# Performance work log

Measured on AMD Instinct MI355X. Metric: run time of the kernel, lower is better.

The kernel has to match this reference:

```python
import jax, jax.numpy as jnp
import numpy as np

V, E, H, D, S = 50257, 512, 512, 1024, 1024


def _gru_final(x_seq, Wih, Whh, bih, bhh):
    """Run a torch-style GRUCell over x_seq [S,E] from h0=0; return final hidden [H]."""
    h_dim = Whh.shape[1]
    gi = x_seq @ Wih.T + bih  # [S,3H] input-side gates, precomputed

    def step(h, g):
        gh = Whh @ h + bhh  # [3H]
        r = jax.nn.sigmoid(g[:h_dim] + gh[:h_dim])
        z = jax.nn.sigmoid(g[h_dim:2 * h_dim] + gh[h_dim:2 * h_dim])
        n = jnp.tanh(g[2 * h_dim:] + r * gh[2 * h_dim:])
        h_new = (1.0 - z) * n + z * h
        return h_new, None

    h_final, _ = jax.lax.scan(step, jnp.zeros((h_dim,), x_seq.dtype), gi)
    return h_final


def _bidir_encode(x_seq, Wih_f, Whh_f, bih_f, bhh_f, Wih_b, Whh_b, bih_b, bhh_b):
    hf = _gru_final(x_seq, Wih_f, Whh_f, bih_f, bhh_f)
    hb = _gru_final(x_seq[::-1], Wih_b, Whh_b, bih_b, bhh_b)
    return jnp.concatenate([hf, hb])  # [2H]


def setup_inputs() -> dict:
    key = jax.random.key(0)
    ks = jax.random.split(key, 32)
    inp = {"sentence": jax.random.randint(ks[0], (S,), 0, V, dtype=jnp.int64)}
    inp["emb"] = jax.random.normal(ks[1], (V, E), jnp.float32) * 0.1
    i = 2
    for pre in ["ctx_f", "ctx_b", "qry_f", "qry_b"]:
        inp[pre + "_Wih"] = jax.random.normal(ks[i], (3 * H, E), jnp.float32) * 0.02; i += 1
        inp[pre + "_Whh"] = jax.random.normal(ks[i], (3 * H, H), jnp.float32) * 0.02; i += 1
        inp[pre + "_bih"] = jax.random.normal(ks[i], (3 * H,), jnp.float32) * 0.02; i += 1
        inp[pre + "_bhh"] = jax.random.normal(ks[i], (3 * H,), jnp.float32) * 0.02; i += 1
    inp["d1_w"] = jax.random.normal(ks[i], (D, 4 * H), jnp.float32) * 0.02; i += 1
    inp["d1_b"] = jnp.zeros((D,), jnp.float32)
    inp["d2_w"] = jax.random.normal(ks[i], (1, D), jnp.float32) * 0.02
    inp["d2_b"] = jnp.zeros((1,), jnp.float32)
    return inp


def reference(sentence, emb,
              ctx_f_Wih, ctx_f_Whh, ctx_f_bih, ctx_f_bhh,
              ctx_b_Wih, ctx_b_Whh, ctx_b_bih, ctx_b_bhh,
              qry_f_Wih, qry_f_Whh, qry_f_bih, qry_f_bhh,
              qry_b_Wih, qry_b_Whh, qry_b_bih, qry_b_bhh,
              d1_w, d1_b, d2_w, d2_b):
    # Embedding lookup (dropout = identity in eval mode)
    x_seq = emb[sentence]  # [S,E]
    ctx = _bidir_encode(x_seq, ctx_f_Wih, ctx_f_Whh, ctx_f_bih, ctx_f_bhh,
                        ctx_b_Wih, ctx_b_Whh, ctx_b_bih, ctx_b_bhh)  # [2H]
    qry = _bidir_encode(x_seq, qry_f_Wih, qry_f_Whh, qry_f_bih, qry_f_bhh,
                        qry_b_Wih, qry_b_Whh, qry_b_bih, qry_b_bhh)  # [2H]
    rep = jnp.concatenate([ctx, qry])  # [4H]
    h1 = jax.nn.relu(rep @ d1_w.T + d1_b)  # [D]
    return jax.nn.sigmoid(h1 @ d2_w.T + d2_b)  # [1]
```

## Files before the change

kernel.cpp:

```cpp
#include <hip/hip_runtime.h>
#include <math.h>

typedef unsigned long long u64;

#define S_LEN 1024
#define E_DIM 512
#define H_DIM 512
#define G3    1536
#define D_DIM 1024

#define NCHAIN 4
#define WPC    32

#define TM 64
#define TN 64
#define BK 32

__global__ __launch_bounds__(256) void gi_gemm_kernel(
    const int* __restrict__ sent, const float* __restrict__ emb,
    const float* __restrict__ Wih0, const float* __restrict__ bih0,
    const float* __restrict__ Wih1, const float* __restrict__ bih1,
    const float* __restrict__ Wih2, const float* __restrict__ bih2,
    const float* __restrict__ Wih3, const float* __restrict__ bih3,
    float* __restrict__ gi)
{
    __shared__ float As[BK][TM + 1];
    __shared__ float Bs[BK][TN + 1];
    __shared__ int   rows[TM];

    const int blocks_t = S_LEN / TM;
    const int blocks_j = G3 / TN;
    int b   = blockIdx.x;
    int p   = b / (blocks_t * blocks_j);
    int rem = b % (blocks_t * blocks_j);
    int bt  = rem / blocks_j;
    int bj  = rem % blocks_j;

    const float* Wih = (p == 0) ? Wih0 : (p == 1) ? Wih1 : (p == 2) ? Wih2 : Wih3;
    const float* bih = (p == 0) ? bih0 : (p == 1) ? bih1 : (p == 2) ? bih2 : bih3;

    int tid = threadIdx.x;
    if (tid < TM) rows[tid] = sent[bt * TM + tid];
    __syncthreads();

    int tt = (tid >> 4) * 4;
    int jj = (tid & 15) * 4;
    float acc[4][4] = {{0.f}};

    int lr = tid >> 2;
    int lc = (tid & 3) * 8;

    for (int k0 = 0; k0 < E_DIM; k0 += BK) {
        const float* asrc = emb + (size_t)rows[lr] * E_DIM + (k0 + lc);
        float4 a0 = *(const float4*)asrc;
        float4 a1 = *(const float4*)(asrc + 4);
        const float* bsrc = Wih + (size_t)(bj * TN + lr) * E_DIM + (k0 + lc);
        float4 b0 = *(const float4*)bsrc;
        float4 b1 = *(const float4*)(bsrc + 4);

        As[lc+0][lr]=a0.x; As[lc+1][lr]=a0.y; As[lc+2][lr]=a0.z; As[lc+3][lr]=a0.w;
        As[lc+4][lr]=a1.x; As[lc+5][lr]=a1.y; As[lc+6][lr]=a1.z; As[lc+7][lr]=a1.w;
        Bs[lc+0][lr]=b0.x; Bs[lc+1][lr]=b0.y; Bs[lc+2][lr]=b0.z; Bs[lc+3][lr]=b0.w;
        Bs[lc+4][lr]=b1.x; Bs[lc+5][lr]=b1.y; Bs[lc+6][lr]=b1.z; Bs[lc+7][lr]=b1.w;
        __syncthreads();

        #pragma unroll
        for (int kk = 0; kk < BK; ++kk) {
            float av[4], bv[4];
            #pragma unroll
            for (int e = 0; e < 4; ++e) { av[e] = As[kk][tt+e]; bv[e] = Bs[kk][jj+e]; }
            #pragma unroll
            for (int i = 0; i < 4; ++i)
                #pragma unroll
                for (int j2 = 0; j2 < 4; ++j2)
                    acc[i][j2] = fmaf(av[i], bv[j2], acc[i][j2]);
        }
        __syncthreads();
    }

    float* gout = gi + (size_t)p * S_LEN * G3;
    int jbase = bj * TN + jj;
    float bb0 = bih[jbase+0], bb1 = bih[jbase+1], bb2 = bih[jbase+2], bb3 = bih[jbase+3];
    #pragma unroll
    for (int i = 0; i < 4; ++i) {
        int t = bt * TM + tt + i;
        float4 v = make_float4(acc[i][0]+bb0, acc[i][1]+bb1, acc[i][2]+bb2, acc[i][3]+bb3);
        *(float4*)(gout + (size_t)t * G3 + jbase) = v;
    }
}

__device__ __forceinline__ float fast_sigmoid(float x) {
    return __builtin_amdgcn_rcpf(1.f + __expf(-x));
}
__device__ __forceinline__ float fast_tanh(float x) {
    return 1.f - 2.f * __builtin_amdgcn_rcpf(1.f + __expf(2.f * x));
}

__global__ __launch_bounds__(256, 1) void gru_scan_kernel(
    const float* __restrict__ Whh0, const float* __restrict__ bhh0,
    const float* __restrict__ Whh1, const float* __restrict__ bhh1,
    const float* __restrict__ Whh2, const float* __restrict__ bhh2,
    const float* __restrict__ Whh3, const float* __restrict__ bhh3,
    const float* __restrict__ gi,
    u64* __restrict__ hpk)
{
    __shared__ float lds_h[2][H_DIM];

    int b = blockIdx.x;
    int c = b / WPC;
    int w = b % WPC;
    const float* Whh = (c==0)?Whh0:(c==1)?Whh1:(c==2)?Whh2:Whh3;
    const float* bhh = (c==0)?bhh0:(c==1)?bhh1:(c==2)?bhh2:bhh3;
    const float* gic = gi + (size_t)c * S_LEN * G3;
    u64* hp = hpk + (size_t)c * 2 * H_DIM;
    const bool fwd = ((c & 1) == 0);

    int tid  = threadIdx.x;
    int wv   = tid >> 6;
    int lane = tid & 63;
    int q    = lane >> 4;
    int r    = lane & 15;
    int base_i = w * 16 + wv * 4;
    int my_i   = base_i + q;
    bool pub   = (r == 0);

    float4 wregv[3][8];
    #pragma unroll
    for (int g = 0; g < 3; ++g) {
        const float* rowp = Whh + (size_t)(g * H_DIM + my_i) * H_DIM;
        #pragma unroll
        for (int k = 0; k < 8; ++k)
            wregv[g][k] = *(const float4*)(rowp + 4 * r + 64 * k);
    }

    float bh_r=0.f, bh_z=0.f, bh_n=0.f;
    float gr=0.f, gz=0.f, gn=0.f;
    if (pub) {
        bh_r = bhh[my_i]; bh_z = bhh[H_DIM + my_i]; bh_n = bhh[2*H_DIM + my_i];
        int t0 = fwd ? 0 : (S_LEN - 1);
        const float* g0 = gic + (size_t)t0 * G3;
        gr = g0[my_i]; gz = g0[H_DIM + my_i]; gn = g0[2*H_DIM + my_i];
    }

    lds_h[0][tid]       = 0.f;
    lds_h[0][tid + 256] = 0.f;

    int s0 = tid, s1 = tid + 256;
    bool own0 = ((s0 >> 4) == w);
    bool own1 = ((s1 >> 4) == w);

    for (int s = 0; s < S_LEN; ++s) {
        int pb = s & 1;
        if (s > 0) {
            const u64* srcp = hp + (size_t)pb * H_DIM;
            bool p0 = own0, p1 = own1;
            while (!(p0 && p1)) {
                if (!p0) {
                    u64 v = __hip_atomic_load(srcp + s0, __ATOMIC_RELAXED, __HIP_MEMORY_SCOPE_AGENT);
                    if ((unsigned)(v >> 32) == (unsigned)s) {
                        lds_h[pb][s0] = __uint_as_float((unsigned)v);
                        p0 = true;
                    }
                }
                if (!p1) {
                    u64 v = __hip_atomic_load(srcp + s1, __ATOMIC_RELAXED, __HIP_MEMORY_SCOPE_AGENT);
                    if ((unsigned)(v >> 32) == (unsigned)s) {
                        lds_h[pb][s1] = __uint_as_float((unsigned)v);
                        p1 = true;
                    }
                }
            }
        }
        __syncthreads();

        float ngr = 0.f, ngz = 0.f, ngn = 0.f;
        if (pub && s + 1 < S_LEN) {
            int tn = fwd ? (s + 1) : (S_LEN - 2 - s);
            const float* gnx = gic + (size_t)tn * G3;
            ngr = gnx[my_i]; ngz = gnx[H_DIM + my_i]; ngn = gnx[2*H_DIM + my_i];
        }

        float hv = lds_h[pb][my_i];

        float4 hfv[8];
        const float* hbase = &lds_h[pb][0];
        #pragma unroll
        for (int k = 0; k < 8; ++k)
            hfv[k] = *(const float4*)(hbase + 4 * r + 64 * k);

        float acc[3];
        #pragma unroll
        for (int g = 0; g < 3; ++g) {
            float a = 0.f;
            #pragma unroll
            for (int k = 0; k < 8; ++k) {
                a = fmaf(wregv[g][k].x, hfv[k].x, a);
                a = fmaf(wregv[g][k].y, hfv[k].y, a);
                a = fmaf(wregv[g][k].z, hfv[k].z, a);
                a = fmaf(wregv[g][k].w, hfv[k].w, a);
            }
            acc[g] = a;
        }
        #pragma unroll
        for (int off = 8; off >= 1; off >>= 1)
            #pragma unroll
            for (int g = 0; g < 3; ++g)
                acc[g] += __shfl_down(acc[g], off, 16);

        if (pub) {
            float rr = fast_sigmoid(gr + acc[0] + bh_r);
            float zz = fast_sigmoid(gz + acc[1] + bh_z);
            float nn = fast_tanh(gn + rr * (acc[2] + bh_n));
            float hn = (1.f - zz) * nn + zz * hv;
            lds_h[pb ^ 1][my_i] = hn;
            union { float f; unsigned u; } cv; cv.f = hn;
            u64 pk = ((u64)(unsigned)(s + 1) << 32) | (u64)cv.u;
            __hip_atomic_store(hp + (size_t)(pb ^ 1) * H_DIM + my_i, pk,
                               __ATOMIC_RELAXED, __HIP_MEMORY_SCOPE_AGENT);
            gr = ngr; gz = ngz; gn = ngn;
        }
    }
}

__global__ __launch_bounds__(256) void dense1_kernel(
    const float* __restrict__ d1w, const float* __restrict__ d1b,
    const u64* __restrict__ hpk, float* __restrict__ h1)
{
    int wv = threadIdx.x >> 6, lane = threadIdx.x & 63;
    int row = blockIdx.x * 4 + wv;
    const float* wr = d1w + (size_t)row * (4 * H_DIM);
    float sum = 0.f;
    #pragma unroll
    for (int q = 0; q < 32; ++q) {
        int j = lane + q * 64;
        int cc = j >> 9;
        float h = __uint_as_float((unsigned)hpk[(size_t)cc * 2 * H_DIM + (j & 511)]);
        sum = fmaf(wr[j], h, sum);
    }
    #pragma unroll
    for (int off = 32; off >= 1; off >>= 1) sum += __shfl_xor(sum, off, 64);
    if (lane == 0) h1[row] = fmaxf(sum + d1b[row], 0.f);
}

__global__ __launch_bounds__(256) void dense2_kernel(
    const float* __restrict__ d2w, const float* __restrict__ d2b,
    const float* __restrict__ h1, float* __restrict__ out)
{
    __shared__ float red[4];
    int tid = threadIdx.x, lane = tid & 63, wv = tid >> 6;
    float sum = 0.f;
    #pragma unroll
    for (int q = 0; q < 4; ++q) { int j = tid + q * 256; sum = fmaf(d2w[j], h1[j], sum); }
    #pragma unroll
    for (int off = 32; off >= 1; off >>= 1) sum += __shfl_xor(sum, off, 64);
    if (lane == 0) red[wv] = sum;
    __syncthreads();
    if (tid == 0) {
        float t = red[0] + red[1] + red[2] + red[3] + d2b[0];
        out[0] = 1.f / (1.f + expf(-t));
    }
}

extern "C" void kernel_launch(void* const* d_in, const int* in_sizes, int n_in,
                              void* d_out, int out_size, void* d_ws, size_t ws_size,
                              hipStream_t stream) {
    const int*   sent = (const int*)d_in[0];
    const float* emb  = (const float*)d_in[1];
    const float* Wih[4], *Whh[4], *bih[4], *bhh[4];
    for (int p = 0; p < 4; ++p) {
        Wih[p] = (const float*)d_in[2 + 4*p + 0];
        Whh[p] = (const float*)d_in[2 + 4*p + 1];
        bih[p] = (const float*)d_in[2 + 4*p + 2];
        bhh[p] = (const float*)d_in[2 + 4*p + 3];
    }
    const float* d1w = (const float*)d_in[18];
    const float* d1b = (const float*)d_in[19];
    const float* d2w = (const float*)d_in[20];
    const float* d2b = (const float*)d_in[21];
    float* out = (float*)d_out;

    float* gi  = (float*)d_ws;
    u64*   hpk = (u64*)((char*)d_ws + (size_t)NCHAIN * S_LEN * G3 * sizeof(float));
    float* h1  = (float*)((char*)hpk + (size_t)NCHAIN * 2 * H_DIM * sizeof(u64));

    gi_gemm_kernel<<<NCHAIN * (S_LEN/TM) * (G3/TN), 256, 0, stream>>>(
        sent, emb,
        Wih[0], bih[0], Wih[1], bih[1], Wih[2], bih[2], Wih[3], bih[3], gi);

    gru_scan_kernel<<<NCHAIN * WPC, 256, 0, stream>>>(
        Whh[0], bhh[0], Whh[1], bhh[1], Whh[2], bhh[2], Whh[3], bhh[3],
        gi, hpk);

    dense1_kernel<<<D_DIM / 4, 256, 0, stream>>>(d1w, d1b, hpk, h1);
    dense2_kernel<<<1, 256, 0, stream>>>(d2w, d2b, h1, out);
}
```

Before: 2.267 ms.

## Fuse input-gate GEMM into the GRU scan, overlapping it with the spin-wait

Removes the separate input-projection GEMM kernel and its large gi workspace. Each scan block now keeps its slice of Wih in registers next to Whh, and computes the input-gate dot products for each step while it polls for the previous hidden state. The embedding row for the next step is prefetched into a double-buffered LDS buffer. In exchange, register pressure doubles (48 float4 weight vectors per thread), each step gains an extra __syncthreads, and the serial scan does more arithmetic per step.

```diff
diff --git a/kernel.cpp b/kernel.cpp
--- a/kernel.cpp
+++ b/kernel.cpp
@@ -12,106 +12,42 @@
 #define NCHAIN 4
 #define WPC    32
 
-#define TM 64
-#define TN 64
-#define BK 32
-
-__global__ __launch_bounds__(256) void gi_gemm_kernel(
-    const int* __restrict__ sent, const float* __restrict__ emb,
-    const float* __restrict__ Wih0, const float* __restrict__ bih0,
-    const float* __restrict__ Wih1, const float* __restrict__ bih1,
-    const float* __restrict__ Wih2, const float* __restrict__ bih2,
-    const float* __restrict__ Wih3, const float* __restrict__ bih3,
-    float* __restrict__ gi)
-{
-    __shared__ float As[BK][TM + 1];
-    __shared__ float Bs[BK][TN + 1];
-    __shared__ int   rows[TM];
-
-    const int blocks_t = S_LEN / TM;
-    const int blocks_j = G3 / TN;
-    int b   = blockIdx.x;
-    int p   = b / (blocks_t * blocks_j);
-    int rem = b % (blocks_t * blocks_j);
-    int bt  = rem / blocks_j;
-    int bj  = rem % blocks_j;
-
-    const float* Wih = (p == 0) ? Wih0 : (p == 1) ? Wih1 : (p == 2) ? Wih2 : Wih3;
-    const float* bih = (p == 0) ? bih0 : (p == 1) ? bih1 : (p == 2) ? bih2 : bih3;
-
-    int tid = threadIdx.x;
-    if (tid < TM) rows[tid] = sent[bt * TM + tid];
-    __syncthreads();
-
-    int tt = (tid >> 4) * 4;
-    int jj = (tid & 15) * 4;
-    float acc[4][4] = {{0.f}};
-
-    int lr = tid >> 2;
-    int lc = (tid & 3) * 8;
-
-    for (int k0 = 0; k0 < E_DIM; k0 += BK) {
-        const float* asrc = emb + (size_t)rows[lr] * E_DIM + (k0 + lc);
-        float4 a0 = *(const float4*)asrc;
-        float4 a1 = *(const float4*)(asrc + 4);
-        const float* bsrc = Wih + (size_t)(bj * TN + lr) * E_DIM + (k0 + lc);
-        float4 b0 = *(const float4*)bsrc;
-        float4 b1 = *(const float4*)(bsrc + 4);
-
-        As[lc+0][lr]=a0.x; As[lc+1][lr]=a0.y; As[lc+2][lr]=a0.z; As[lc+3][lr]=a0.w;
-        As[lc+4][lr]=a1.x; As[lc+5][lr]=a1.y; As[lc+6][lr]=a1.z; As[lc+7][lr]=a1.w;
-        Bs[lc+0][lr]=b0.x; Bs[lc+1][lr]=b0.y; Bs[lc+2][lr]=b0.z; Bs[lc+3][lr]=b0.w;
-        Bs[lc+4][lr]=b1.x; Bs[lc+5][lr]=b1.y; Bs[lc+6][lr]=b1.z; Bs[lc+7][lr]=b1.w;
-        __syncthreads();
-
-        #pragma unroll
-        for (int kk = 0; kk < BK; ++kk) {
-            float av[4], bv[4];
-            #pragma unroll
-            for (int e = 0; e < 4; ++e) { av[e] = As[kk][tt+e]; bv[e] = Bs[kk][jj+e]; }
-            #pragma unroll
-            for (int i = 0; i < 4; ++i)
-                #pragma unroll
-                for (int j2 = 0; j2 < 4; ++j2)
-                    acc[i][j2] = fmaf(av[i], bv[j2], acc[i][j2]);
-        }
-        __syncthreads();
-    }
-
-    float* gout = gi + (size_t)p * S_LEN * G3;
-    int jbase = bj * TN + jj;
-    float bb0 = bih[jbase+0], bb1 = bih[jbase+1], bb2 = bih[jbase+2], bb3 = bih[jbase+3];
-    #pragma unroll
-    for (int i = 0; i < 4; ++i) {
-        int t = bt * TM + tt + i;
-        float4 v = make_float4(acc[i][0]+bb0, acc[i][1]+bb1, acc[i][2]+bb2, acc[i][3]+bb3);
-        *(float4*)(gout + (size_t)t * G3 + jbase) = v;
-    }
-}
-
 __device__ __forceinline__ float fast_sigmoid(float x) {
     return __builtin_amdgcn_rcpf(1.f + __expf(-x));
 }
 __device__ __forceinline__ float fast_tanh(float x) {
     return 1.f - 2.f * __builtin_amdgcn_rcpf(1.f + __expf(2.f * x));
 }
-
-__global__ __launch_bounds__(256, 1) void gru_scan_kernel(
-    const float* __restrict__ Whh0, const float* __restrict__ bhh0,
-    const float* __restrict__ Whh1, const float* __restrict__ bhh1,
-    const float* __restrict__ Whh2, const float* __restrict__ bhh2,
-    const float* __restrict__ Whh3, const float* __restrict__ bhh3,
-    const float* __restrict__ gi,
+__device__ __forceinline__ float dot4(float4 a, float4 b, float acc) {
+    acc = fmaf(a.x, b.x, acc);
+    acc = fmaf(a.y, b.y, acc);
+    acc = fmaf(a.z, b.z, acc);
+    acc = fmaf(a.w, b.w, acc);
+    return acc;
+}
+
+__global__ __launch_bounds__(256, 1) void gru_scan_fused_kernel(
+    const int* __restrict__ sent, const float* __restrict__ emb,
+    const float* __restrict__ Wih0, const float* __restrict__ Whh0,
+    const float* __restrict__ bih0, const float* __restrict__ bhh0,
+    const float* __restrict__ Wih1, const float* __restrict__ Whh1,
+    const float* __restrict__ bih1, const float* __restrict__ bhh1,
+    const float* __restrict__ Wih2, const float* __restrict__ Whh2,
+    const float* __restrict__ bih2, const float* __restrict__ bhh2,
+    const float* __restrict__ Wih3, const float* __restrict__ Whh3,
+    const float* __restrict__ bih3, const float* __restrict__ bhh3,
     u64* __restrict__ hpk)
 {
     __shared__ float lds_h[2][H_DIM];
+    __shared__ float lds_x[2][E_DIM];
 
     int b = blockIdx.x;
     int c = b / WPC;
     int w = b % WPC;
+    const float* Wih = (c==0)?Wih0:(c==1)?Wih1:(c==2)?Wih2:Wih3;
     const float* Whh = (c==0)?Whh0:(c==1)?Whh1:(c==2)?Whh2:Whh3;
+    const float* bih = (c==0)?bih0:(c==1)?bih1:(c==2)?bih2:bih3;
     const float* bhh = (c==0)?bhh0:(c==1)?bhh1:(c==2)?bhh2:bhh3;
-    const float* gic = gi + (size_t)c * S_LEN * G3;
     u64* hp = hpk + (size_t)c * 2 * H_DIM;
     const bool fwd = ((c & 1) == 0);
 
@@ -124,26 +60,35 @@
     int my_i   = base_i + q;
     bool pub   = (r == 0);
 
-    float4 wregv[3][8];
+    float4 whr[3][8], wir[3][8];
     #pragma unroll
     for (int g = 0; g < 3; ++g) {
-        const float* rowp = Whh + (size_t)(g * H_DIM + my_i) * H_DIM;
+        const float* hrow = Whh + (size_t)(g * H_DIM + my_i) * H_DIM;
+        const float* irow = Wih + (size_t)(g * H_DIM + my_i) * E_DIM;
         #pragma unroll
-        for (int k = 0; k < 8; ++k)
-            wregv[g][k] = *(const float4*)(rowp + 4 * r + 64 * k);
+        for (int k = 0; k < 8; ++k) {
+            whr[g][k] = *(const float4*)(hrow + 4 * r + 64 * k);
+            wir[g][k] = *(const float4*)(irow + 4 * r + 64 * k);
+        }
     }
 
     float bh_r=0.f, bh_z=0.f, bh_n=0.f;
-    float gr=0.f, gz=0.f, gn=0.f;
+    float bi_r=0.f, bi_z=0.f, bi_n=0.f;
     if (pub) {
         bh_r = bhh[my_i]; bh_z = bhh[H_DIM + my_i]; bh_n = bhh[2*H_DIM + my_i];
-        int t0 = fwd ? 0 : (S_LEN - 1);
-        const float* g0 = gic + (size_t)t0 * G3;
-        gr = g0[my_i]; gz = g0[H_DIM + my_i]; gn = g0[2*H_DIM + my_i];
+        bi_r = bih[my_i]; bi_z = bih[H_DIM + my_i]; bi_n = bih[2*H_DIM + my_i];
     }
 
     lds_h[0][tid]       = 0.f;
     lds_h[0][tid + 256] = 0.f;
+    {
+        int t0 = fwd ? 0 : (S_LEN - 1);
+        int row0 = sent[t0];
+        if (tid < 128)
+            *(float4*)&lds_x[0][tid * 4] =
+                *(const float4*)(emb + (size_t)row0 * E_DIM + tid * 4);
+    }
+    __syncthreads();
 
     int s0 = tid, s1 = tid + 256;
     bool own0 = ((s0 >> 4) == w);
@@ -151,74 +96,87 @@
 
     for (int s = 0; s < S_LEN; ++s) {
         int pb = s & 1;
+        const float* xb = &lds_x[pb][0];
+        float ea0 = 0.f, ea1 = 0.f, ea2 = 0.f;
+        int ac = 0;
+
         if (s > 0) {
             const u64* srcp = hp + (size_t)pb * H_DIM;
             bool p0 = own0, p1 = own1;
             while (!(p0 && p1)) {
-                if (!p0) {
-                    u64 v = __hip_atomic_load(srcp + s0, __ATOMIC_RELAXED, __HIP_MEMORY_SCOPE_AGENT);
-                    if ((unsigned)(v >> 32) == (unsigned)s) {
-                        lds_h[pb][s0] = __uint_as_float((unsigned)v);
-                        p0 = true;
-                    }
+                u64 v0 = 0, v1 = 0;
+                if (!p0) v0 = __hip_atomic_load(srcp + s0, __ATOMIC_RELAXED, __HIP_MEMORY_SCOPE_AGENT);
+                if (!p1) v1 = __hip_atomic_load(srcp + s1, __ATOMIC_RELAXED, __HIP_MEMORY_SCOPE_AGENT);
+                if (ac < 8) {
+                    float4 xv = *(const float4*)(xb + 4 * r + 64 * ac);
+                    ea0 = dot4(wir[0][ac], xv, ea0);
+                    ea1 = dot4(wir[1][ac], xv, ea1);
+                    ea2 = dot4(wir[2][ac], xv, ea2);
+                    ++ac;
                 }
-                if (!p1) {
-                    u64 v = __hip_atomic_load(srcp + s1, __ATOMIC_RELAXED, __HIP_MEMORY_SCOPE_AGENT);
-                    if ((unsigned)(v >> 32) == (unsigned)s) {
-                        lds_h[pb][s1] = __uint_as_float((unsigned)v);
-                        p1 = true;
-                    }
+                if (!p0 && (unsigned)(v0 >> 32) == (unsigned)s) {
+                    lds_h[pb][s0] = __uint_as_float((unsigned)v0);
+                    p0 = true;
+                }
+                if (!p1 && (unsigned)(v1 >> 32) == (unsigned)s) {
+                    lds_h[pb][s1] = __uint_as_float((unsigned)v1);
+                    p1 = true;
                 }
             }
         }
+        for (; ac < 8; ++ac) {
+            float4 xv = *(const float4*)(xb + 4 * r + 64 * ac);
+            ea0 = dot4(wir[0][ac], xv, ea0);
+            ea1 = dot4(wir[1][ac], xv, ea1);
+            ea2 = dot4(wir[2][ac], xv, ea2);
+        }
         __syncthreads();
 
-        float ngr = 0.f, ngz = 0.f, ngn = 0.f;
-        if (pub && s + 1 < S_LEN) {
+        float4 xpre = make_float4(0.f, 0.f, 0.f, 0.f);
+        bool do_pre = (tid < 128) && (s + 1 < S_LEN);
+        if (do_pre) {
             int tn = fwd ? (s + 1) : (S_LEN - 2 - s);
-            const float* gnx = gic + (size_t)tn * G3;
-            ngr = gnx[my_i]; ngz = gnx[H_DIM + my_i]; ngn = gnx[2*H_DIM + my_i];
+            int rown = sent[tn];
+            xpre = *(const float4*)(emb + (size_t)rown * E_DIM + tid * 4);
         }
 
         float hv = lds_h[pb][my_i];
 
-        float4 hfv[8];
-        const float* hbase = &lds_h[pb][0];
+        float ha0 = 0.f, ha1 = 0.f, ha2 = 0.f;
+        const float* hb = &lds_h[pb][0];
         #pragma unroll
-        for (int k = 0; k < 8; ++k)
-            hfv[k] = *(const float4*)(hbase + 4 * r + 64 * k);
-
-        float acc[3];
+        for (int k = 0; k < 8; ++k) {
+            float4 hfv = *(const float4*)(hb + 4 * r + 64 * k);
+            ha0 = dot4(whr[0][k], hfv, ha0);
+            ha1 = dot4(whr[1][k], hfv, ha1);
+            ha2 = dot4(whr[2][k], hfv, ha2);
+        }
+
+        float red0 = ea0 + ha0;
+        float red1 = ea1 + ha1;
+        float red2 = ea2;
+        float red3 = ha2;
         #pragma unroll
-        for (int g = 0; g < 3; ++g) {
-            float a = 0.f;
-            #pragma unroll
-            for (int k = 0; k < 8; ++k) {
-                a = fmaf(wregv[g][k].x, hfv[k].x, a);
-                a = fmaf(wregv[g][k].y, hfv[k].y, a);
-                a = fmaf(wregv[g][k].z, hfv[k].z, a);
-                a = fmaf(wregv[g][k].w, hfv[k].w, a);
-            }
-            acc[g] = a;
-        }
-        #pragma unroll
-        for (int off = 8; off >= 1; off >>= 1)
-            #pragma unroll
-            for (int g = 0; g < 3; ++g)
-                acc[g] += __shfl_down(acc[g], off, 16);
+        for (int off = 8; off >= 1; off >>= 1) {
+            red0 += __shfl_down(red0, off, 16);
+            red1 += __shfl_down(red1, off, 16);
+            red2 += __shfl_down(red2, off, 16);
+            red3 += __shfl_down(red3, off, 16);
+        }
 
         if (pub) {
-            float rr = fast_sigmoid(gr + acc[0] + bh_r);
-            float zz = fast_sigmoid(gz + acc[1] + bh_z);
-            float nn = fast_tanh(gn + rr * (acc[2] + bh_n));
+            float rr = fast_sigmoid(red0 + bi_r + bh_r);
+            float zz = fast_sigmoid(red1 + bi_z + bh_z);
+            float nn = fast_tanh((red2 + bi_n) + rr * (red3 + bh_n));
             float hn = (1.f - zz) * nn + zz * hv;
             lds_h[pb ^ 1][my_i] = hn;
             union { float f; unsigned u; } cv; cv.f = hn;
             u64 pk = ((u64)(unsigned)(s + 1) << 32) | (u64)cv.u;
             __hip_atomic_store(hp + (size_t)(pb ^ 1) * H_DIM + my_i, pk,
                                __ATOMIC_RELAXED, __HIP_MEMORY_SCOPE_AGENT);
-            gr = ngr; gz = ngz; gn = ngn;
-        }
+        }
+        if (do_pre) *(float4*)&lds_x[pb ^ 1][tid * 4] = xpre;
+        __syncthreads();
     }
 }
 
@@ -279,17 +237,16 @@
     const float* d2b = (const float*)d_in[21];
     float* out = (float*)d_out;
 
-    float* gi  = (float*)d_ws;
     u64*   hpk = (u64*)((char*)d_ws + (size_t)NCHAIN * S_LEN * G3 * sizeof(float));
     float* h1  = (float*)((char*)hpk + (size_t)NCHAIN * 2 * H_DIM * sizeof(u64));
 
-    gi_gemm_kernel<<<NCHAIN * (S_LEN/TM) * (G3/TN), 256, 0, stream>>>(
+    gru_scan_fused_kernel<<<NCHAIN * WPC, 256, 0, stream>>>(
         sent, emb,
-        Wih[0], bih[0], Wih[1], bih[1], Wih[2], bih[2], Wih[3], bih[3], gi);
-
-    gru_scan_kernel<<<NCHAIN * WPC, 256, 0, stream>>>(
-        Whh[0], bhh[0], Whh[1], bhh[1], Whh[2], bhh[2], Whh[3], bhh[3],
-        gi, hpk);
+        Wih[0], Whh[0], bih[0], bhh[0],
+        Wih[1], Whh[1], bih[1], bhh[1],
+        Wih[2], Whh[2], bih[2], bhh[2],
+        Wih[3], Whh[3], bih[3], bhh[3],
+        hpk);
 
     dense1_kernel<<<D_DIM / 4, 256, 0, stream>>>(d1w, d1b, hpk, h1);
     dense2_kernel<<<1, 256, 0, stream>>>(d2w, d2b, h1, out);
```

Result: slower. 4.589 ms (+102.4%).

## Pad hidden-state publish slots and enlarge gi GEMM tiles to 128x128

Applied to the files above, without the earlier changes.

Each published hidden-state slot in the GRU scan is spread out by a stride `ss` (up to 32 u64s, limited by workspace size), so neighbouring elements no longer share cache lines. This is meant to reduce contention between polling readers and publishing writers across workgroups. The input-gate GEMM is also retiled from 64x64 with BK=32 to 128x128 with BK=16, giving each thread an 8x8 micro-tile for more register reuse. The cost is higher register pressure and fewer GEMM blocks, and the padding makes the dense layer's hidden-state reads strided.

```diff
diff --git a/kernel.cpp b/kernel.cpp
--- a/kernel.cpp
+++ b/kernel.cpp
@@ -12,9 +12,9 @@
 #define NCHAIN 4
 #define WPC    32
 
-#define TM 64
-#define TN 64
-#define BK 32
+#define TMG 128
+#define TNG 128
+#define BKG 16
 
 __global__ __launch_bounds__(256) void gi_gemm_kernel(
     const int* __restrict__ sent, const float* __restrict__ emb,
@@ -24,12 +24,12 @@
     const float* __restrict__ Wih3, const float* __restrict__ bih3,
     float* __restrict__ gi)
 {
-    __shared__ float As[BK][TM + 1];
-    __shared__ float Bs[BK][TN + 1];
-    __shared__ int   rows[TM];
-
-    const int blocks_t = S_LEN / TM;
-    const int blocks_j = G3 / TN;
+    __shared__ float As[BKG][TMG + 1];
+    __shared__ float Bs[BKG][TNG + 1];
+    __shared__ int   rows[TMG];
+
+    const int blocks_t = S_LEN / TMG;
+    const int blocks_j = G3 / TNG;
     int b   = blockIdx.x;
     int p   = b / (blocks_t * blocks_j);
     int rem = b % (blocks_t * blocks_j);
@@ -40,21 +40,21 @@
     const float* bih = (p == 0) ? bih0 : (p == 1) ? bih1 : (p == 2) ? bih2 : bih3;
 
     int tid = threadIdx.x;
-    if (tid < TM) rows[tid] = sent[bt * TM + tid];
+    if (tid < TMG) rows[tid] = sent[bt * TMG + tid];
     __syncthreads();
 
-    int tt = (tid >> 4) * 4;
-    int jj = (tid & 15) * 4;
-    float acc[4][4] = {{0.f}};
-
-    int lr = tid >> 2;
-    int lc = (tid & 3) * 8;
-
-    for (int k0 = 0; k0 < E_DIM; k0 += BK) {
+    int tt4 = (tid >> 4) * 4;
+    int jj4 = (tid & 15) * 4;
+    float acc[8][8] = {{0.f}};
+
+    int lr = tid >> 1;
+    int lc = (tid & 1) * 8;
+
+    for (int k0 = 0; k0 < E_DIM; k0 += BKG) {
         const float* asrc = emb + (size_t)rows[lr] * E_DIM + (k0 + lc);
         float4 a0 = *(const float4*)asrc;
         float4 a1 = *(const float4*)(asrc + 4);
-        const float* bsrc = Wih + (size_t)(bj * TN + lr) * E_DIM + (k0 + lc);
+        const float* bsrc = Wih + (size_t)(bj * TNG + lr) * E_DIM + (k0 + lc);
         float4 b0 = *(const float4*)bsrc;
         float4 b1 = *(const float4*)(bsrc + 4);
 
@@ -65,27 +65,36 @@
         __syncthreads();
 
         #pragma unroll
-        for (int kk = 0; kk < BK; ++kk) {
-            float av[4], bv[4];
+        for (int kk = 0; kk < BKG; ++kk) {
+            float av[8], bv[8];
             #pragma unroll
-            for (int e = 0; e < 4; ++e) { av[e] = As[kk][tt+e]; bv[e] = Bs[kk][jj+e]; }
+            for (int e = 0; e < 4; ++e) {
+                av[e]   = As[kk][tt4 + e];
+                av[4+e] = As[kk][64 + tt4 + e];
+                bv[e]   = Bs[kk][jj4 + e];
+                bv[4+e] = Bs[kk][64 + jj4 + e];
+            }
             #pragma unroll
-            for (int i = 0; i < 4; ++i)
+            for (int i = 0; i < 8; ++i)
                 #pragma unroll
-                for (int j2 = 0; j2 < 4; ++j2)
+                for (int j2 = 0; j2 < 8; ++j2)
                     acc[i][j2] = fmaf(av[i], bv[j2], acc[i][j2]);
         }
         __syncthreads();
     }
 
     float* gout = gi + (size_t)p * S_LEN * G3;
-    int jbase = bj * TN + jj;
-    float bb0 = bih[jbase+0], bb1 = bih[jbase+1], bb2 = bih[jbase+2], bb3 = bih[jbase+3];
-    #pragma unroll
-    for (int i = 0; i < 4; ++i) {
-        int t = bt * TM + tt + i;
-        float4 v = make_float4(acc[i][0]+bb0, acc[i][1]+bb1, acc[i][2]+bb2, acc[i][3]+bb3);
-        *(float4*)(gout + (size_t)t * G3 + jbase) = v;
+    int jb0 = bj * TNG + jj4;
+    int jb1 = jb0 + 64;
+    float c00 = bih[jb0+0], c01 = bih[jb0+1], c02 = bih[jb0+2], c03 = bih[jb0+3];
+    float c10 = bih[jb1+0], c11 = bih[jb1+1], c12 = bih[jb1+2], c13 = bih[jb1+3];
+    #pragma unroll
+    for (int i = 0; i < 8; ++i) {
+        int t = bt * TMG + ((i < 4) ? (tt4 + i) : (64 + tt4 + (i - 4)));
+        float4 v0 = make_float4(acc[i][0]+c00, acc[i][1]+c01, acc[i][2]+c02, acc[i][3]+c03);
+        float4 v1 = make_float4(acc[i][4]+c10, acc[i][5]+c11, acc[i][6]+c12, acc[i][7]+c13);
+        *(float4*)(gout + (size_t)t * G3 + jb0) = v0;
+        *(float4*)(gout + (size_t)t * G3 + jb1) = v1;
     }
 }
 
@@ -102,7 +111,8 @@
     const float* __restrict__ Whh2, const float* __restrict__ bhh2,
     const float* __restrict__ Whh3, const float* __restrict__ bhh3,
     const float* __restrict__ gi,
-    u64* __restrict__ hpk)
+    u64* __restrict__ hpk,
+    int ss)
 {
     __shared__ float lds_h[2][H_DIM];
 
@@ -112,7 +122,8 @@
     const float* Whh = (c==0)?Whh0:(c==1)?Whh1:(c==2)?Whh2:Whh3;
     const float* bhh = (c==0)?bhh0:(c==1)?bhh1:(c==2)?bhh2:bhh3;
     const float* gic = gi + (size_t)c * S_LEN * G3;
-    u64* hp = hpk + (size_t)c * 2 * H_DIM;
+    u64* hp = hpk + (size_t)c * 2 * H_DIM * ss;
+    const size_t par = (size_t)H_DIM * ss;
     const bool fwd = ((c & 1) == 0);
 
     int tid  = threadIdx.x;
@@ -148,22 +159,25 @@
     int s0 = tid, s1 = tid + 256;
     bool own0 = ((s0 >> 4) == w);
     bool own1 = ((s1 >> 4) == w);
+    u64* slotA = hp + (size_t)s0 * ss;
+    u64* slotB = hp + (size_t)s1 * ss;
+    u64* pubp  = hp + (size_t)my_i * ss;
 
     for (int s = 0; s < S_LEN; ++s) {
         int pb = s & 1;
+        size_t poff = pb ? par : 0;
         if (s > 0) {
-            const u64* srcp = hp + (size_t)pb * H_DIM;
             bool p0 = own0, p1 = own1;
             while (!(p0 && p1)) {
                 if (!p0) {
-                    u64 v = __hip_atomic_load(srcp + s0, __ATOMIC_RELAXED, __HIP_MEMORY_SCOPE_AGENT);
+                    u64 v = __hip_atomic_load(slotA + poff, __ATOMIC_RELAXED, __HIP_MEMORY_SCOPE_AGENT);
                     if ((unsigned)(v >> 32) == (unsigned)s) {
                         lds_h[pb][s0] = __uint_as_float((unsigned)v);
                         p0 = true;
                     }
                 }
                 if (!p1) {
-                    u64 v = __hip_atomic_load(srcp + s1, __ATOMIC_RELAXED, __HIP_MEMORY_SCOPE_AGENT);
+                    u64 v = __hip_atomic_load(slotB + poff, __ATOMIC_RELAXED, __HIP_MEMORY_SCOPE_AGENT);
                     if ((unsigned)(v >> 32) == (unsigned)s) {
                         lds_h[pb][s1] = __uint_as_float((unsigned)v);
                         p1 = true;
@@ -215,7 +229,7 @@
             lds_h[pb ^ 1][my_i] = hn;
             union { float f; unsigned u; } cv; cv.f = hn;
             u64 pk = ((u64)(unsigned)(s + 1) << 32) | (u64)cv.u;
-            __hip_atomic_store(hp + (size_t)(pb ^ 1) * H_DIM + my_i, pk,
+            __hip_atomic_store(pubp + (pb ? 0 : par), pk,
                                __ATOMIC_RELAXED, __HIP_MEMORY_SCOPE_AGENT);
             gr = ngr; gz = ngz; gn = ngn;
         }
@@ -224,7 +238,7 @@
 
 __global__ __launch_bounds__(256) void dense1_kernel(
     const float* __restrict__ d1w, const float* __restrict__ d1b,
-    const u64* __restrict__ hpk, float* __restrict__ h1)
+    const u64* __restrict__ hpk, float* __restrict__ h1, int ss)
 {
     int wv = threadIdx.x >> 6, lane = threadIdx.x & 63;
     int row = blockIdx.x * 4 + wv;
@@ -234,7 +248,8 @@
     for (int q = 0; q < 32; ++q) {
         int j = lane + q * 64;
         int cc = j >> 9;
-        float h = __uint_as_float((unsigned)hpk[(size_t)cc * 2 * H_DIM + (j & 511)]);
+        u64 v = hpk[((size_t)cc * 2 * H_DIM + (j & 511)) * ss];
+        float h = __uint_as_float((unsigned)v);
         sum = fmaf(wr[j], h, sum);
     }
     #pragma unroll
@@ -279,18 +294,26 @@
     const float* d2b = (const float*)d_in[21];
     float* out = (float*)d_out;
 
+    size_t gi_bytes = (size_t)NCHAIN * S_LEN * G3 * sizeof(float);
+    size_t h1_bytes = (size_t)D_DIM * sizeof(float);
+    size_t base = gi_bytes + h1_bytes;
+    size_t avail = (ws_size > base) ? (ws_size - base) : 0;
+    int ss = 1;
+    while (ss < 32 && (size_t)NCHAIN * 2 * H_DIM * (size_t)(ss * 2) * sizeof(u64) <= avail)
+        ss *= 2;
+
     float* gi  = (float*)d_ws;
-    u64*   hpk = (u64*)((char*)d_ws + (size_t)NCHAIN * S_LEN * G3 * sizeof(float));
-    float* h1  = (float*)((char*)hpk + (size_t)NCHAIN * 2 * H_DIM * sizeof(u64));
-
-    gi_gemm_kernel<<<NCHAIN * (S_LEN/TM) * (G3/TN), 256, 0, stream>>>(
+    float* h1  = (float*)((char*)d_ws + gi_bytes);
+    u64*   hpk = (u64*)((char*)d_ws + base);
+
+    gi_gemm_kernel<<<NCHAIN * (S_LEN/TMG) * (G3/TNG), 256, 0, stream>>>(
         sent, emb,
         Wih[0], bih[0], Wih[1], bih[1], Wih[2], bih[2], Wih[3], bih[3], gi);
 
     gru_scan_kernel<<<NCHAIN * WPC, 256, 0, stream>>>(
         Whh[0], bhh[0], Whh[1], bhh[1], Whh[2], bhh[2], Whh[3], bhh[3],
-        gi, hpk);
-
-    dense1_kernel<<<D_DIM / 4, 256, 0, stream>>>(d1w, d1b, hpk, h1);
+        gi, hpk, ss);
+
+    dense1_kernel<<<D_DIM / 4, 256, 0, stream>>>(d1w, d1b, hpk, h1, ss);
     dense2_kernel<<<1, 256, 0, stream>>>(d2w, d2b, h1, out);
 }
```

New measurement: 2.742 ms. 21.0% more time.

## Poll hidden state directly into registers, dropping LDS staging and block barrier

Applied to the files above, without the earlier changes.

Each lane now atomically loads the 32 tagged hidden-state values it needs for its dot product straight from global memory and spins until all carry the current step tag. This removes the LDS copy of h and the per-step __syncthreads, so each wavefront proceeds on its own. Each lane's own previous hidden value is kept in a register. The cost is redundant global polling: each of the 4 quads in a wave, and each wave, loads the same 32 values. This adds L2 traffic and spin loads, and a retry reloads all 32 entries.

```diff
diff --git a/kernel.cpp b/kernel.cpp
--- a/kernel.cpp
+++ b/kernel.cpp
@@ -95,6 +95,13 @@
 __device__ __forceinline__ float fast_tanh(float x) {
     return 1.f - 2.f * __builtin_amdgcn_rcpf(1.f + __expf(2.f * x));
 }
+__device__ __forceinline__ float dot4(float4 a, float4 b, float acc) {
+    acc = fmaf(a.x, b.x, acc);
+    acc = fmaf(a.y, b.y, acc);
+    acc = fmaf(a.z, b.z, acc);
+    acc = fmaf(a.w, b.w, acc);
+    return acc;
+}
 
 __global__ __launch_bounds__(256, 1) void gru_scan_kernel(
     const float* __restrict__ Whh0, const float* __restrict__ bhh0,
@@ -104,8 +111,6 @@
     const float* __restrict__ gi,
     u64* __restrict__ hpk)
 {
-    __shared__ float lds_h[2][H_DIM];
-
     int b = blockIdx.x;
     int c = b / WPC;
     int w = b % WPC;
@@ -142,36 +147,10 @@
         gr = g0[my_i]; gz = g0[H_DIM + my_i]; gn = g0[2*H_DIM + my_i];
     }
 
-    lds_h[0][tid]       = 0.f;
-    lds_h[0][tid + 256] = 0.f;
-
-    int s0 = tid, s1 = tid + 256;
-    bool own0 = ((s0 >> 4) == w);
-    bool own1 = ((s1 >> 4) == w);
+    float hv_reg = 0.f;
 
     for (int s = 0; s < S_LEN; ++s) {
         int pb = s & 1;
-        if (s > 0) {
-            const u64* srcp = hp + (size_t)pb * H_DIM;
-            bool p0 = own0, p1 = own1;
-            while (!(p0 && p1)) {
-                if (!p0) {
-                    u64 v = __hip_atomic_load(srcp + s0, __ATOMIC_RELAXED, __HIP_MEMORY_SCOPE_AGENT);
-                    if ((unsigned)(v >> 32) == (unsigned)s) {
-                        lds_h[pb][s0] = __uint_as_float((unsigned)v);
-                        p0 = true;
-                    }
-                }
-                if (!p1) {
-                    u64 v = __hip_atomic_load(srcp + s1, __ATOMIC_RELAXED, __HIP_MEMORY_SCOPE_AGENT);
-                    if ((unsigned)(v >> 32) == (unsigned)s) {
-                        lds_h[pb][s1] = __uint_as_float((unsigned)v);
-                        p1 = true;
-                    }
-                }
-            }
-        }
-        __syncthreads();
 
         float ngr = 0.f, ngz = 0.f, ngn = 0.f;
         if (pub && s + 1 < S_LEN) {
@@ -180,39 +159,48 @@
             ngr = gnx[my_i]; ngz = gnx[H_DIM + my_i]; ngn = gnx[2*H_DIM + my_i];
         }
 
-        float hv = lds_h[pb][my_i];
-
-        float4 hfv[8];
-        const float* hbase = &lds_h[pb][0];
-        #pragma unroll
-        for (int k = 0; k < 8; ++k)
-            hfv[k] = *(const float4*)(hbase + 4 * r + 64 * k);
-
-        float acc[3];
-        #pragma unroll
-        for (int g = 0; g < 3; ++g) {
-            float a = 0.f;
+        float acc0 = 0.f, acc1 = 0.f, acc2 = 0.f;
+        if (s > 0) {
+            const u64* srcp = hp + (size_t)pb * H_DIM + 4 * r;
+            u64 sv[32];
+            for (;;) {
+                #pragma unroll
+                for (int k = 0; k < 8; ++k)
+                    #pragma unroll
+                    for (int e = 0; e < 4; ++e)
+                        sv[k * 4 + e] = __hip_atomic_load(srcp + 64 * k + e,
+                                                          __ATOMIC_RELAXED, __HIP_MEMORY_SCOPE_AGENT);
+                unsigned ok = 1u;
+                #pragma unroll
+                for (int i = 0; i < 32; ++i)
+                    ok &= ((unsigned)(sv[i] >> 32) == (unsigned)s) ? 1u : 0u;
+                if (ok) break;
+            }
             #pragma unroll
             for (int k = 0; k < 8; ++k) {
-                a = fmaf(wregv[g][k].x, hfv[k].x, a);
-                a = fmaf(wregv[g][k].y, hfv[k].y, a);
-                a = fmaf(wregv[g][k].z, hfv[k].z, a);
-                a = fmaf(wregv[g][k].w, hfv[k].w, a);
+                float4 hfv = make_float4(
+                    __uint_as_float((unsigned)sv[k*4+0]),
+                    __uint_as_float((unsigned)sv[k*4+1]),
+                    __uint_as_float((unsigned)sv[k*4+2]),
+                    __uint_as_float((unsigned)sv[k*4+3]));
+                acc0 = dot4(wregv[0][k], hfv, acc0);
+                acc1 = dot4(wregv[1][k], hfv, acc1);
+                acc2 = dot4(wregv[2][k], hfv, acc2);
             }
-            acc[g] = a;
         }
         #pragma unroll
-        for (int off = 8; off >= 1; off >>= 1)
-            #pragma unroll
-            for (int g = 0; g < 3; ++g)
-                acc[g] += __shfl_down(acc[g], off, 16);
+        for (int off = 8; off >= 1; off >>= 1) {
+            acc0 += __shfl_down(acc0, off, 16);
+            acc1 += __shfl_down(acc1, off, 16);
+            acc2 += __shfl_down(acc2, off, 16);
+        }
 
         if (pub) {
-            float rr = fast_sigmoid(gr + acc[0] + bh_r);
-            float zz = fast_sigmoid(gz + acc[1] + bh_z);
-            float nn = fast_tanh(gn + rr * (acc[2] + bh_n));
-            float hn = (1.f - zz) * nn + zz * hv;
-            lds_h[pb ^ 1][my_i] = hn;
+            float rr = fast_sigmoid(gr + acc0 + bh_r);
+            float zz = fast_sigmoid(gz + acc1 + bh_z);
+            float nn = fast_tanh(gn + rr * (acc2 + bh_n));
+            float hn = (1.f - zz) * nn + zz * hv_reg;
+            hv_reg = hn;
             union { float f; unsigned u; } cv; cv.f = hn;
             u64 pk = ((u64)(unsigned)(s + 1) << 32) | (u64)cv.u;
             __hip_atomic_store(hp + (size_t)(pb ^ 1) * H_DIM + my_i, pk,
```

New measurement: 3.295 ms. 1.45x slower.
